# Kernel optimization log

Measured on AMD Instinct MI355X. Metric: run time of the kernel, lower is better.

## Reference

```python
import jax, jax.numpy as jnp
import numpy as np

N, C = 32768, 128
G, L = 64, 512
E = 524288
D_STATE, D_CONV, EXPAND = 16, 4, 2
D_INNER = EXPAND * C
DT_RANK = (C + 15) // 16  # ceil(d_model/16) = 8
EPS = 1e-5


def batch_norm(x, gamma, beta):
    # training-mode BatchNorm1d (batch statistics), eps=1e-5
    m = jnp.mean(x, axis=0)
    v = jnp.var(x, axis=0)
    return gamma * (x - m) * jax.lax.rsqrt(v + EPS) + beta


def mamba(h, in_W, conv_w, conv_b, xproj_W, dt_W, dt_b, A_log, Dp, out_W):
    # h: (G, L, C) dense-batched node features
    xz = h @ in_W                                   # (G, L, 2*D_INNER)
    xi, z = jnp.split(xz, 2, axis=-1)
    # causal depthwise conv1d (pad left d_conv-1), then SiLU
    xp = jnp.pad(xi, ((0, 0), (D_CONV - 1, 0), (0, 0)))
    xc = conv_b + sum(xp[:, k:k + L, :] * conv_w[:, k] for k in range(D_CONV))
    xc = jax.nn.silu(xc)                            # (G, L, D_INNER)
    proj = xc @ xproj_W                             # (G, L, DT_RANK + 2*D_STATE)
    dt_raw, Bm, Cm = jnp.split(proj, [DT_RANK, DT_RANK + D_STATE], axis=-1)
    dt = jax.nn.softplus(dt_raw @ dt_W + dt_b)      # (G, L, D_INNER)
    A = -jnp.exp(A_log)                             # (D_INNER, D_STATE)

    def step(hst, inp):
        dt_t, B_t, C_t, x_t = inp                   # (G,DI),(G,DS),(G,DS),(G,DI)
        dA = jnp.exp(dt_t[:, :, None] * A)          # (G, D_INNER, D_STATE)
        hst = hst * dA + (dt_t * x_t)[:, :, None] * B_t[:, None, :]
        y = jnp.einsum('gds,gs->gd', hst, C_t)
        return hst, y

    xs = (jnp.swapaxes(dt, 0, 1), jnp.swapaxes(Bm, 0, 1),
          jnp.swapaxes(Cm, 0, 1), jnp.swapaxes(xc, 0, 1))
    h0 = jnp.zeros((G, D_INNER, D_STATE), dt.dtype)
    _, ys = jax.lax.scan(step, h0, xs)              # ys: (L, G, D_INNER)
    y = jnp.swapaxes(ys, 0, 1) + xc * Dp
    y = y * jax.nn.silu(z)
    return y @ out_W                                # (G, L, C)


def setup_inputs() -> dict:
    key = jax.random.key(0)
    ks = jax.random.split(key, 16)
    s = 0.02
    rn = lambda k, shp: jax.random.normal(k, shp, jnp.float32) * s
    inp = {
        'x': jax.random.normal(ks[0], (N, C), jnp.float32),
        'edge_index': jax.random.randint(ks[1], (2, E), 0, N),
        'batch': jnp.arange(N) // L,  # 64 equal-size, sorted graphs
        # GraphConv (add-aggr): out = lin_rel(sum_j x_j) + lin_root(x)
        'W_root': rn(ks[2], (C, C)),
        'W_rel': rn(ks[3], (C, C)),
        'b_rel': jnp.zeros((C,), jnp.float32),
        # norm1/2/3 (BatchNorm1d)
        'n1_g': jnp.ones((C,), jnp.float32), 'n1_b': jnp.zeros((C,), jnp.float32),
        'n2_g': jnp.ones((C,), jnp.float32), 'n2_b': jnp.zeros((C,), jnp.float32),
        'n3_g': jnp.ones((C,), jnp.float32), 'n3_b': jnp.zeros((C,), jnp.float32),
        # MLP: BN -> Linear(C,2C) -> GELU -> BN -> Linear(2C,C)
        'mlp_bn1_g': jnp.ones((C,), jnp.float32), 'mlp_bn1_b': jnp.zeros((C,), jnp.float32),
        'mlp_W1': rn(ks[4], (C, 2 * C)), 'mlp_b1': jnp.zeros((2 * C,), jnp.float32),
        'mlp_bn2_g': jnp.ones((2 * C,), jnp.float32), 'mlp_bn2_b': jnp.zeros((2 * C,), jnp.float32),
        'mlp_W2': rn(ks[5], (2 * C, C)), 'mlp_b2': jnp.zeros((C,), jnp.float32),
        # Mamba params
        'in_W': rn(ks[6], (C, 2 * D_INNER)),
        'conv_w': rn(ks[7], (D_INNER, D_CONV)),
        'conv_b': jnp.zeros((D_INNER,), jnp.float32),
        'xproj_W': rn(ks[8], (D_INNER, DT_RANK + 2 * D_STATE)),
        'dt_W': rn(ks[9], (DT_RANK, D_INNER)),
        'dt_b': rn(ks[10], (D_INNER,)),
        'A_log': jnp.log(jnp.tile(jnp.arange(1, D_STATE + 1, dtype=jnp.float32), (D_INNER, 1))),
        'Dp': jnp.ones((D_INNER,), jnp.float32),
        'out_W': rn(ks[11], (D_INNER, C)),
    }
    return inp


def reference(x, edge_index, batch, W_root, W_rel, b_rel,
              n1_g, n1_b, n2_g, n2_b, n3_g, n3_b,
              mlp_bn1_g, mlp_bn1_b, mlp_W1, mlp_b1,
              mlp_bn2_g, mlp_bn2_b, mlp_W2, mlp_b2,
              in_W, conv_w, conv_b, xproj_W, dt_W, dt_b, A_log, Dp, out_W):
    src, dst = edge_index[0], edge_index[1]
    # conv branch (GraphConv, sum aggregation) + residual + norm1
    agg = jax.ops.segment_sum(x[src], dst, num_segments=N)
    h1 = agg @ W_rel + b_rel + x @ W_root + x
    h1 = batch_norm(h1, n1_g, n1_b)
    # mamba branch: to_dense_batch == reshape (batch = arange(N)//L, mask all-True)
    hd = x.reshape(G, L, C)
    y = mamba(hd, in_W, conv_w, conv_b, xproj_W, dt_W, dt_b, A_log, Dp, out_W).reshape(N, C)
    h2 = batch_norm(y + x, n2_g, n2_b)
    out = h1 + h2
    # gated MLP with internal batch norms (dropout is identity in eval)
    m = batch_norm(out, mlp_bn1_g, mlp_bn1_b) @ mlp_W1 + mlp_b1
    m = jax.nn.gelu(m, approximate=False)
    m = batch_norm(m, mlp_bn2_g, mlp_bn2_b) @ mlp_W2 + mlp_b2
    out = out + m
    return batch_norm(out, n3_g, n3_b)
```

## Files before the change

kernel.cpp:

```cpp
#include <hip/hip_runtime.h>


#define NROWS 32768
#define CDIM  128
#define EDGES 524288
#define GL    512
#define SCH   32
#define NCH   (GL / SCH)

typedef short s16x8 __attribute__((ext_vector_type(8)));
typedef float f32x4 __attribute__((ext_vector_type(4)));

__device__ __forceinline__ unsigned short f2bf(float f)
{
    unsigned u = __float_as_uint(f);
    u += 0x7FFF + ((u >> 16) & 1);
    return (unsigned short)(u >> 16);
}

__device__ __forceinline__ float bf2f(unsigned short u)
{
    return __uint_as_float((unsigned)u << 16);
}

__device__ __forceinline__ unsigned cvt_pk_bf16(float lo, float hi)
{
    unsigned r;
    asm("v_cvt_pk_bf16_f32 %0, %1, %2" : "=v"(r) : "v"(lo), "v"(hi));
    return r;
}

__device__ __forceinline__ float exp2_fast(float x)
{
    float r;
    asm("v_exp_f32 %0, %1" : "=v"(r) : "v"(x));
    return r;
}

__global__ __launch_bounds__(256) void k_hist(const int* __restrict__ ei,
                                              int* __restrict__ deg)
{
    const int e = blockIdx.x * 1024 + threadIdx.x * 4;
    const int4 d4 = *(const int4*)&ei[EDGES + e];
    atomicAdd(&deg[d4.x], 1);
    atomicAdd(&deg[d4.y], 1);
    atomicAdd(&deg[d4.z], 1);
    atomicAdd(&deg[d4.w], 1);
}

__global__ __launch_bounds__(1024) void k_scanidx(const int* __restrict__ deg,
                                                  int* __restrict__ base,
                                                  int* __restrict__ cursor)
{
    __shared__ int ps[1024];
    const int tid = threadIdx.x;
    int loc[32];
    int s = 0;
#pragma unroll
    for (int i = 0; i < 32; ++i) { loc[i] = deg[tid * 32 + i]; s += loc[i]; }
    ps[tid] = s;
    __syncthreads();
    for (int off = 1; off < 1024; off <<= 1) {
        int v = (tid >= off) ? ps[tid - off] : 0;
        __syncthreads();
        ps[tid] += v;
        __syncthreads();
    }
    int run = tid ? ps[tid - 1] : 0;
#pragma unroll
    for (int i = 0; i < 32; ++i) {
        base[tid * 32 + i] = run;
        cursor[tid * 32 + i] = run;
        run += loc[i];
    }
    if (tid == 0) base[32768] = EDGES;
}

__global__ __launch_bounds__(256) void k_fill(const int* __restrict__ ei,
                                              int* __restrict__ cursor,
                                              int* __restrict__ srcs)
{
    const int e = blockIdx.x * 1024 + threadIdx.x * 4;
    const int4 s4 = *(const int4*)&ei[e];
    const int4 d4 = *(const int4*)&ei[EDGES + e];
    int p;
    p = atomicAdd(&cursor[d4.x], 1); srcs[p] = s4.x;
    p = atomicAdd(&cursor[d4.y], 1); srcs[p] = s4.y;
    p = atomicAdd(&cursor[d4.z], 1); srcs[p] = s4.z;
    p = atomicAdd(&cursor[d4.w], 1); srcs[p] = s4.w;
}

__global__ __launch_bounds__(256) void k_gather(const float* __restrict__ x,
                                                const int* __restrict__ base,
                                                const int* __restrict__ srcs,
                                                float* __restrict__ agg)
{
    const int node = blockIdx.x * 4 + (threadIdx.x >> 6);
    const int lane = threadIdx.x & 63;
    const int b0 = base[node], b1 = base[node + 1];
    float2 a0 = make_float2(0.f, 0.f), a1 = make_float2(0.f, 0.f);
    int i = b0;
    for (; i + 2 <= b1; i += 2) {
        const int s0 = srcs[i], s1 = srcs[i + 1];
        const float2 v0 = *(const float2*)&x[(size_t)s0 * 128 + lane * 2];
        const float2 v1 = *(const float2*)&x[(size_t)s1 * 128 + lane * 2];
        a0.x += v0.x; a0.y += v0.y;
        a1.x += v1.x; a1.y += v1.y;
    }
    if (i < b1) {
        const int s0 = srcs[i];
        const float2 v0 = *(const float2*)&x[(size_t)s0 * 128 + lane * 2];
        a0.x += v0.x; a0.y += v0.y;
    }
    a0.x += a1.x; a0.y += a1.y;
    *(float2*)&agg[(size_t)node * 128 + lane * 2] = a0;
}

__global__ __launch_bounds__(256) void k_prepw5(
    const float* __restrict__ Wa, unsigned short* __restrict__ Ta,
    const float* __restrict__ Wb, unsigned short* __restrict__ Tb,
    const float* __restrict__ Wc, unsigned short* __restrict__ Tc,
    const float* __restrict__ Wd, unsigned short* __restrict__ Td,
    const float* __restrict__ We, unsigned short* __restrict__ Te)
{
    const int idx = blockIdx.x * 256 + threadIdx.x;
    const float* W; unsigned short* T; int rel, ks, N;
    if (idx < 16384)       { W = Wa; T = Ta; rel = idx;          ks = 7; N = 128; }
    else if (idx < 32768)  { W = Wb; T = Tb; rel = idx - 16384;  ks = 7; N = 128; }
    else if (idx < 98304)  { W = Wc; T = Tc; rel = idx - 32768;  ks = 7; N = 512; }
    else if (idx < 108544) { W = Wd; T = Td; rel = idx - 98304;  ks = 8; N = 40;  }
    else                   { W = We; T = Te; rel = idx - 108544; ks = 8; N = 128; }
    const int K = 1 << ks;
    const int n = rel >> ks, k = rel & (K - 1);
    T[rel] = f2bf(W[(size_t)k * N + n]);
}

template<bool DUAL, int ACT, bool STAT, bool ABF, bool OBF>
__global__ __launch_bounds__(256)
void gemm_mfma(const void* __restrict__ A0, const unsigned short* __restrict__ W0T,
               const void* __restrict__ A1p, const unsigned short* __restrict__ W1Tp,
               int M, int N, int K, int ldo,
               const float* __restrict__ bias,
               const float* __restrict__ resid, int ldr,
               void* __restrict__ outp,
               float* __restrict__ sumP, float* __restrict__ sqP)
{
    __shared__ __align__(16) unsigned short As[64 * 72];
    __shared__ __align__(16) unsigned short Bs[64 * 72];
    __shared__ float sB[2][64];

    const int tid = threadIdx.x;
    const int m0 = blockIdx.x * 64;
    const int n0 = blockIdx.y * 64;

    const int sr = tid >> 2;
    const int sk = (tid & 3) * 16;

    const int w  = tid >> 6, l = tid & 63;
    const int wr = (w >> 1) * 32, wc = (w & 1) * 32;
    const int fr = l & 15;
    const int fk = (l >> 4) * 8;

    f32x4 acc[2][2];
#pragma unroll
    for (int i = 0; i < 2; ++i)
#pragma unroll
        for (int j = 0; j < 2; ++j) acc[i][j] = (f32x4){0.f, 0.f, 0.f, 0.f};

    const int npass = DUAL ? 2 : 1;
    for (int pass = 0; pass < npass; ++pass) {
        const void* A = (DUAL && pass) ? A1p : A0;
        const unsigned short* WT = (DUAL && pass) ? W1Tp : W0T;
        for (int k0 = 0; k0 < K; k0 += 64) {
            if (ABF) {
                const unsigned short* ap =
                    (const unsigned short*)A + (size_t)(m0 + sr) * K + k0 + sk;
                *(uint4*)&As[sr * 72 + sk]     = *(const uint4*)(ap);
                *(uint4*)&As[sr * 72 + sk + 8] = *(const uint4*)(ap + 8);
            } else {
                const float* ap = (const float*)A + (size_t)(m0 + sr) * K + k0 + sk;
                float4 v0 = *(const float4*)(ap);
                float4 v1 = *(const float4*)(ap + 4);
                float4 v2 = *(const float4*)(ap + 8);
                float4 v3 = *(const float4*)(ap + 12);
                uint4 pa, pb;
                pa.x = cvt_pk_bf16(v0.x, v0.y); pa.y = cvt_pk_bf16(v0.z, v0.w);
                pa.z = cvt_pk_bf16(v1.x, v1.y); pa.w = cvt_pk_bf16(v1.z, v1.w);
                pb.x = cvt_pk_bf16(v2.x, v2.y); pb.y = cvt_pk_bf16(v2.z, v2.w);
                pb.z = cvt_pk_bf16(v3.x, v3.y); pb.w = cvt_pk_bf16(v3.z, v3.w);
                *(uint4*)&As[sr * 72 + sk]     = pa;
                *(uint4*)&As[sr * 72 + sk + 8] = pb;
            }
            {
                const int nn = n0 + sr;
                if (nn < N) {
                    const unsigned short* wp = WT + (size_t)nn * K + k0 + sk;
                    uint4 w0 = *(const uint4*)(wp);
                    uint4 w1 = *(const uint4*)(wp + 8);
                    *(uint4*)&Bs[sr * 72 + sk]     = w0;
                    *(uint4*)&Bs[sr * 72 + sk + 8] = w1;
                } else {
                    uint4 z = make_uint4(0, 0, 0, 0);
                    *(uint4*)&Bs[sr * 72 + sk]     = z;
                    *(uint4*)&Bs[sr * 72 + sk + 8] = z;
                }
            }
            __syncthreads();
#pragma unroll
            for (int ks = 0; ks < 2; ++ks) {
                s16x8 a0 = *(const s16x8*)&As[(wr + fr     ) * 72 + ks * 32 + fk];
                s16x8 a1 = *(const s16x8*)&As[(wr + 16 + fr) * 72 + ks * 32 + fk];
                s16x8 b0 = *(const s16x8*)&Bs[(wc + fr     ) * 72 + ks * 32 + fk];
                s16x8 b1 = *(const s16x8*)&Bs[(wc + 16 + fr) * 72 + ks * 32 + fk];
                acc[0][0] = __builtin_amdgcn_mfma_f32_16x16x32_bf16(a0, b0, acc[0][0], 0, 0, 0);
                acc[0][1] = __builtin_amdgcn_mfma_f32_16x16x32_bf16(a0, b1, acc[0][1], 0, 0, 0);
                acc[1][0] = __builtin_amdgcn_mfma_f32_16x16x32_bf16(a1, b0, acc[1][0], 0, 0, 0);
                acc[1][1] = __builtin_amdgcn_mfma_f32_16x16x32_bf16(a1, b1, acc[1][1], 0, 0, 0);
            }
            __syncthreads();
        }
    }

    const int orow = (l >> 4) * 4;
    float cs[2] = {0.f, 0.f}, cq[2] = {0.f, 0.f};
#pragma unroll
    for (int mt = 0; mt < 2; ++mt) {
#pragma unroll
        for (int nt = 0; nt < 2; ++nt) {
            const int cg = n0 + wc + nt * 16 + fr;
            if (cg < N) {
                const float bv = bias ? bias[cg] : 0.f;
#pragma unroll
                for (int r = 0; r < 4; ++r) {
                    const int rg = m0 + wr + mt * 16 + orow + r;
                    float v = acc[mt][nt][r] + bv;
                    if (resid) v += resid[(size_t)rg * ldr + cg];
                    if (ACT == 1)
                        v = 0.5f * v * (1.f + erff(v * 0.7071067811865475f));
                    if (OBF)
                        ((unsigned short*)outp)[(size_t)rg * ldo + cg] = f2bf(v);
                    else
                        ((float*)outp)[(size_t)rg * ldo + cg] = v;
                    if (STAT) { cs[nt] += v; cq[nt] += v * v; }
                }
            }
        }
    }
    if (STAT) {
        if (tid < 64) { sB[0][tid] = 0.f; sB[1][tid] = 0.f; }
        __syncthreads();
#pragma unroll
        for (int nt = 0; nt < 2; ++nt) {
            atomicAdd(&sB[0][wc + nt * 16 + fr], cs[nt]);
            atomicAdd(&sB[1][wc + nt * 16 + fr], cq[nt]);
        }
        __syncthreads();
        if (tid < 64 && (n0 + tid) < N) {
            atomicAdd(&sumP[n0 + tid], sB[0][tid]);
            atomicAdd(&sqP[n0 + tid],  sB[1][tid]);
        }
    }
}

__global__ __launch_bounds__(256) void k_conv(const unsigned short* __restrict__ xz,
                                              const float* __restrict__ cw,
                                              const float* __restrict__ cb,
                                              unsigned short* __restrict__ xc)
{
    const int r = blockIdx.x;
    const int l = r & (GL - 1);
    const int d = threadIdx.x;
    float4 w4 = *(const float4*)&cw[d * 4];
    const float taps[4] = {w4.x, w4.y, w4.z, w4.w};
    float acc = cb[d];
#pragma unroll
    for (int k = 0; k < 4; ++k) {
        int ll = l - 3 + k;
        if (ll >= 0) acc += bf2f(xz[(size_t)(r - 3 + k) * 512 + d]) * taps[k];
    }
    float s = 1.f / (1.f + __expf(-acc));
    xc[(size_t)r * 256 + d] = f2bf(acc * s);
}

__global__ __launch_bounds__(256) void k_dtbc(const float* __restrict__ proj,
                                              const float* __restrict__ dt_W,
                                              const float* __restrict__ dt_b,
                                              unsigned short* __restrict__ dtb,
                                              float* __restrict__ Bc,
                                              float* __restrict__ Cc)
{
    __shared__ float dtWS[8 * 256];
    __shared__ float dt_bS[256];
    __shared__ float projS[32 * 8];
    const int tid = threadIdx.x;
    const int r0 = blockIdx.x * 32;
    for (int i = tid; i < 2048; i += 256) dtWS[i] = dt_W[i];
    dt_bS[tid] = dt_b[tid];
    projS[tid] = proj[(size_t)(r0 + (tid >> 3)) * 40 + (tid & 7)];
    __syncthreads();

    const int c = tid;
    for (int rr = 0; rr < 32; ++rr) {
        float acc = dt_bS[c];
        const float* pr = &projS[rr * 8];
#pragma unroll
        for (int q = 0; q < 8; ++q) acc += pr[q] * dtWS[q * 256 + c];
        float e  = exp2_fast(-fabsf(acc) * 1.4426950408f);
        float sp = fmaxf(acc, 0.f) + 0.6931471806f * __log2f(1.f + e);
        dtb[(size_t)(r0 + rr) * 256 + c] = f2bf(sp);
    }
    for (int e2 = tid; e2 < 1024; e2 += 256) {
        int rr = e2 >> 5, cc = e2 & 31;
        float v = proj[(size_t)(r0 + rr) * 40 + 8 + cc];
        if (cc < 16) Bc[(size_t)(r0 + rr) * 16 + cc] = v;
        else         Cc[(size_t)(r0 + rr) * 16 + cc - 16] = v;
    }
}

__device__ __forceinline__ float dpp_add8(float x)
{
    float y = x;
    int t;
    t = __builtin_amdgcn_update_dpp(0, __float_as_int(y), 0xB1, 0xF, 0xF, true);
    y += __int_as_float(t);
    t = __builtin_amdgcn_update_dpp(0, __float_as_int(y), 0x4E, 0xF, 0xF, true);
    y += __int_as_float(t);
    t = __builtin_amdgcn_update_dpp(0, __float_as_int(y), 0x141, 0xF, 0xF, true);
    y += __int_as_float(t);
    return y;
}

__global__ __launch_bounds__(256) void k_scan(
    const unsigned short* __restrict__ dtb,
    const unsigned short* __restrict__ xcb,
    const unsigned short* __restrict__ xzb,
    const float* __restrict__ Bb, const float* __restrict__ Cb,
    const float* __restrict__ A_log, const float* __restrict__ Dp,
    unsigned short* __restrict__ yg)
{
    __shared__ __align__(16) float lds[2 * 3456 + 32 * 36];

    const int g    = blockIdx.x >> 3;
    const int dblk = blockIdx.x & 7;
    const int tid  = threadIdx.x;
    const int lane = tid & 63;
    const int dl   = (tid >> 6) * 8 + (lane >> 3);
    const int sp   = lane & 7;
    const int d0   = dblk * 32;
    const int d    = d0 + dl;
    const size_t rbase = (size_t)g * GL;

    const int sdd = tid & 31, stq = tid >> 5;
    const int sbt = tid >> 4, sbi = tid & 15;
    const int szt = tid >> 3, szi = tid & 7;

    const float L2E = 1.44269504088896f;
    const float aA0 = -__expf(A_log[d * 16 + 2 * sp]) * L2E;
    const float aA1 = -__expf(A_log[d * 16 + 2 * sp + 1]) * L2E;
    const float Dpd = Dp[d];
    float h0 = 0.f, h1 = 0.f;

    float rdt[4], rxc[4];
    float rB0, rB1, rC0, rC1;
    ushort4 rz, zcur;

    {
        const size_t r0 = rbase;
#pragma unroll
        for (int j = 0; j < 4; ++j) {
            rdt[j] = bf2f(dtb[(r0 + stq * 4 + j) * 256 + d0 + sdd]);
            rxc[j] = bf2f(xcb[(r0 + stq * 4 + j) * 256 + d0 + sdd]);
        }
        rz  = *(const ushort4*)&xzb[(r0 + szt) * 512 + 256 + d0 + szi * 4];
        rB0 = Bb[(r0 + sbt) * 16 + sbi];
        rB1 = Bb[(r0 + sbt + 16) * 16 + sbi];
        rC0 = Cb[(r0 + sbt) * 16 + sbi];
        rC1 = Cb[(r0 + sbt + 16) * 16 + sbi];
    }
    zcur = rz;

    float* ygL = lds + 2 * 3456;

    for (int c = 0; c < NCH; ++c) {
        float* buf = lds + (c & 1) * 3456;
        *(float4*)&buf[sdd * 36 + stq * 4] =
            make_float4(rdt[0], rdt[1], rdt[2], rdt[3]);
        *(float4*)&buf[1152 + sdd * 36 + stq * 4] =
            make_float4(rxc[0], rxc[1], rxc[2], rxc[3]);
        buf[2304 + sbi * 36 + sbt]      = rB0;
        buf[2304 + sbi * 36 + sbt + 16] = rB1;
        buf[2880 + sbi * 36 + sbt]      = rC0;
        buf[2880 + sbi * 36 + sbt + 16] = rC1;
        zcur = rz;
        __syncthreads();

        if (c + 1 < NCH) {
            const size_t r0 = rbase + (size_t)(c + 1) * SCH;
#pragma unroll
            for (int j = 0; j < 4; ++j) {
                rdt[j] = bf2f(dtb[(r0 + stq * 4 + j) * 256 + d0 + sdd]);
                rxc[j] = bf2f(xcb[(r0 + stq * 4 + j) * 256 + d0 + sdd]);
            }
            rz  = *(const ushort4*)&xzb[(r0 + szt) * 512 + 256 + d0 + szi * 4];
            rB0 = Bb[(r0 + sbt) * 16 + sbi];
            rB1 = Bb[(r0 + sbt + 16) * 16 + sbi];
            rC0 = Cb[(r0 + sbt) * 16 + sbi];
            rC1 = Cb[(r0 + sbt + 16) * 16 + sbi];
        }

        const float* pdt = buf + dl * 36;
        const float* pxc = buf + 1152 + dl * 36;
        const float* pB0 = buf + 2304 + (2 * sp) * 36;
        const float* pB1 = buf + 2304 + (2 * sp + 1) * 36;
        const float* pC0 = buf + 2880 + (2 * sp) * 36;
        const float* pC1 = buf + 2880 + (2 * sp + 1) * 36;
        float yk[4] = {0.f, 0.f, 0.f, 0.f};
#pragma unroll
        for (int t4 = 0; t4 < 8; ++t4) {
            const float4 dt4 = *(const float4*)&pdt[t4 * 4];
            const float4 xc4 = *(const float4*)&pxc[t4 * 4];
            const float4 B04 = *(const float4*)&pB0[t4 * 4];
            const float4 B14 = *(const float4*)&pB1[t4 * 4];
            const float4 C04 = *(const float4*)&pC0[t4 * 4];
            const float4 C14 = *(const float4*)&pC1[t4 * 4];
#define SSTEP(J)                                                            \
            {                                                               \
                const float dt = ((const float*)&dt4)[J];                   \
                const float xc = ((const float*)&xc4)[J];                   \
                const float dtx = dt * xc;                                  \
                h0 = h0 * exp2_fast(dt * aA0) + dtx * ((const float*)&B04)[J]; \
                h1 = h1 * exp2_fast(dt * aA1) + dtx * ((const float*)&B14)[J]; \
                float yv = h0 * ((const float*)&C04)[J]                     \
                         + h1 * ((const float*)&C14)[J];                    \
                yv = dpp_add8(yv);                                          \
                yv = fmaf(xc, Dpd, yv);                                     \
                const int tt = t4 * 4 + (J);                                \
                yk[t4 >> 1] = (sp == (tt & 7)) ? yv : yk[t4 >> 1];          \
            }
            SSTEP(0) SSTEP(1) SSTEP(2) SSTEP(3)
#undef SSTEP
        }
#pragma unroll
        for (int k = 0; k < 4; ++k)
            ygL[(k * 8 + sp) * 36 + dl] = yk[k];
        __syncthreads();

        {
            const size_t rr0 = rbase + (size_t)c * SCH;
            float4 y4 = *(const float4*)&ygL[szt * 36 + szi * 4];
            float z0 = bf2f(zcur.x), z1 = bf2f(zcur.y);
            float z2 = bf2f(zcur.z), z3 = bf2f(zcur.w);
            float o0 = y4.x * (z0 / (1.f + __expf(-z0)));
            float o1 = y4.y * (z1 / (1.f + __expf(-z1)));
            float o2 = y4.z * (z2 / (1.f + __expf(-z2)));
            float o3 = y4.w * (z3 / (1.f + __expf(-z3)));
            uint2 packed;
            packed.x = cvt_pk_bf16(o0, o1);
            packed.y = cvt_pk_bf16(o2, o3);
            *(uint2*)&yg[(rr0 + szt) * 256 + d0 + szi * 4] = packed;
        }
    }
}

__global__ __launch_bounds__(256) void k_add(const float* __restrict__ h1p,
                                             const float* __restrict__ p2,
                                             const float* __restrict__ st,
                                             const float* __restrict__ g1,
                                             const float* __restrict__ be1,
                                             const float* __restrict__ g2,
                                             const float* __restrict__ be2,
                                             float* __restrict__ outp,
                                             float* __restrict__ sumP,
                                             float* __restrict__ sqP)
{
    const int c = threadIdx.x & 127, half = threadIdx.x >> 7;
    const float inv = 1.f / 32768.f;
    const float m1 = st[c] * inv, v1 = st[128 + c] * inv - m1 * m1;
    const float a1 = g1[c] * rsqrtf(v1 + 1e-5f), b1 = be1[c] - m1 * a1;
    const float m2 = st[256 + c] * inv, v2 = st[384 + c] * inv - m2 * m2;
    const float a2 = g2[c] * rsqrtf(v2 + 1e-5f), b2 = be2[c] - m2 * a2;

    const int rbase = blockIdx.x * 64 + half * 32;
    float s = 0.f, q = 0.f;
    for (int i = 0; i < 32; ++i) {
        size_t idx = (size_t)(rbase + i) * 128 + c;
        float v = h1p[idx] * a1 + b1 + p2[idx] * a2 + b2;
        outp[idx] = v; s += v; q += v * v;
    }
    __shared__ float sh[2][2][128];
    sh[0][half][c] = s; sh[1][half][c] = q;
    __syncthreads();
    if (threadIdx.x < 128) {
        atomicAdd(&sumP[c], sh[0][0][c] + sh[0][1][c]);
        atomicAdd(&sqP[c],  sh[1][0][c] + sh[1][1][c]);
    }
}

__global__ __launch_bounds__(128) void k_fold1(
    const float* __restrict__ sumP, const float* __restrict__ sqP,
    const float* __restrict__ gam, const float* __restrict__ bet,
    const float* __restrict__ W1, const float* __restrict__ b1in,
    unsigned short* __restrict__ W1eT, float* __restrict__ b1e)
{
    __shared__ float red[128];
    const int n = blockIdx.x, k = threadIdx.x;
    const float inv = 1.f / 32768.f;
    const float m = sumP[k] * inv, v = sqP[k] * inv - m * m;
    const float a = gam[k] * rsqrtf(v + 1e-5f), bs = bet[k] - m * a;
    const float wv = W1[k * 256 + n];
    W1eT[n * 128 + k] = f2bf(a * wv);
    red[k] = bs * wv;
    __syncthreads();
    for (int s = 64; s > 0; s >>= 1) {
        if (k < s) red[k] += red[k + s];
        __syncthreads();
    }
    if (k == 0) b1e[n] = red[0] + b1in[n];
}

__global__ __launch_bounds__(256) void k_fold2(
    const float* __restrict__ sumP, const float* __restrict__ sqP,
    const float* __restrict__ gam, const float* __restrict__ bet,
    const float* __restrict__ W2, const float* __restrict__ b2in,
    unsigned short* __restrict__ W2eT, float* __restrict__ b2e)
{
    __shared__ float red[256];
    const int n = blockIdx.x, k = threadIdx.x;
    const float inv = 1.f / 32768.f;
    const float m = sumP[k] * inv, v = sqP[k] * inv - m * m;
    const float a = gam[k] * rsqrtf(v + 1e-5f), bs = bet[k] - m * a;
    const float wv = W2[k * 128 + n];
    W2eT[n * 256 + k] = f2bf(a * wv);
    red[k] = bs * wv;
    __syncthreads();
    for (int s = 128; s > 0; s >>= 1) {
        if (k < s) red[k] += red[k + s];
        __syncthreads();
    }
    if (k == 0) b2e[n] = red[0] + b2in[n];
}

__global__ __launch_bounds__(256) void k_bn3(const float* __restrict__ out2,
                                             const float* __restrict__ sumP,
                                             const float* __restrict__ sqP,
                                             const float* __restrict__ gam,
                                             const float* __restrict__ bet,
                                             float* __restrict__ dout)
{
    const int cq = (threadIdx.x & 31) * 4;
    const int rw = threadIdx.x >> 5;
    const float inv = 1.f / 32768.f;
    float a[4], b[4];
#pragma unroll
    for (int j = 0; j < 4; ++j) {
        float m = sumP[cq + j] * inv, v = sqP[cq + j] * inv - m * m;
        a[j] = gam[cq + j] * rsqrtf(v + 1e-5f);
        b[j] = bet[cq + j] - m * a[j];
    }
    const int r0 = blockIdx.x * 128 + rw;
#pragma unroll 4
    for (int k = 0; k < 16; ++k) {
        const size_t r = r0 + k * 8;
        float4 v = *(const float4*)&out2[r * 128 + cq];
        v.x = v.x * a[0] + b[0]; v.y = v.y * a[1] + b[1];
        v.z = v.z * a[2] + b[2]; v.w = v.w * a[3] + b[3];
        *(float4*)&dout[r * 128 + cq] = v;
    }
}

extern "C" void kernel_launch(void* const* d_in, const int* in_sizes, int n_in,
                              void* d_out, int out_size, void* d_ws, size_t ws_size,
                              hipStream_t stream)
{
    (void)in_sizes; (void)n_in; (void)out_size; (void)ws_size;
    const float* x      = (const float*)d_in[0];
    const int*   ei     = (const int*)d_in[1];
    const float* W_root = (const float*)d_in[3];
    const float* W_rel  = (const float*)d_in[4];
    const float* b_rel  = (const float*)d_in[5];
    const float* n1_g = (const float*)d_in[6],  *n1_b = (const float*)d_in[7];
    const float* n2_g = (const float*)d_in[8],  *n2_b = (const float*)d_in[9];
    const float* n3_g = (const float*)d_in[10], *n3_b = (const float*)d_in[11];
    const float* m1_g = (const float*)d_in[12], *m1_b = (const float*)d_in[13];
    const float* W1   = (const float*)d_in[14], *b1   = (const float*)d_in[15];
    const float* m2_g = (const float*)d_in[16], *m2_b = (const float*)d_in[17];
    const float* W2   = (const float*)d_in[18], *b2   = (const float*)d_in[19];
    const float* in_W   = (const float*)d_in[20];
    const float* conv_w = (const float*)d_in[21], *conv_b = (const float*)d_in[22];
    const float* xproj_W= (const float*)d_in[23];
    const float* dt_W   = (const float*)d_in[24], *dt_b = (const float*)d_in[25];
    const float* A_log  = (const float*)d_in[26], *Dp   = (const float*)d_in[27];
    const float* out_W  = (const float*)d_in[28];

    float* ws = (float*)d_ws;
    float* st  = ws;
    float* b1e = ws + 8192;
    float* b2e = ws + 8448;
    unsigned short* wsh   = (unsigned short*)(ws + 8704);
    unsigned short* WrelT  = wsh;
    unsigned short* WrootT = wsh + 16384;
    unsigned short* inWT   = wsh + 32768;
    unsigned short* xprojT = wsh + 98304;
    unsigned short* outWT  = wsh + 108544;
    unsigned short* W1eT   = wsh + 141312;
    unsigned short* W2eT   = wsh + 174080;
    float* big  = ws + 112640;
    float* agg  = big;
    float* p2   = agg;
    float* h1p  = big + 4194304;
    unsigned short* xz16  = (unsigned short*)(big + 8388608);
    unsigned short* xc16  = (unsigned short*)(big + 16777216);
    float* proj = big + 20971520;
    unsigned short* dtb16 = (unsigned short*)(big + 22282240);
    unsigned short* yg16  = dtb16;
    float* Bc   = big + 26476544;
    float* Cc   = big + 27000832;
    float* outb = big + 27525120;
    float* out2 = big + 31719424;
    unsigned short* g16   = (unsigned short*)(big + 35913728);

    int* ideg   = (int*)h1p;
    int* ibase  = ideg + 32768;
    int* icur   = ideg + 65552;
    int* isrcs  = ideg + 98320;

    hipMemsetAsync(st, 0, 2048 * sizeof(float), stream);
    hipMemsetAsync(ideg, 0, 32768 * sizeof(int), stream);

    k_prepw5<<<552, 256, 0, stream>>>(W_rel, WrelT, W_root, WrootT,
                                      in_W, inWT, xproj_W, xprojT,
                                      out_W, outWT);

    k_hist<<<512, 256, 0, stream>>>(ei, ideg);
    k_scanidx<<<1, 1024, 0, stream>>>(ideg, ibase, icur);
    k_fill<<<512, 256, 0, stream>>>(ei, icur, isrcs);
    k_gather<<<8192, 256, 0, stream>>>(x, ibase, isrcs, agg);

    gemm_mfma<true, 0, true, false, false><<<dim3(512, 2), 256, 0, stream>>>(
        agg, WrelT, x, WrootT, NROWS, 128, 128, 128,
        b_rel, x, 128, h1p, st + 0, st + 128);
    gemm_mfma<false, 0, false, false, true><<<dim3(512, 8), 256, 0, stream>>>(
        x, inWT, nullptr, nullptr, NROWS, 512, 128, 512,
        nullptr, nullptr, 0, xz16, nullptr, nullptr);
    k_conv<<<32768, 256, 0, stream>>>(xz16, conv_w, conv_b, xc16);
    gemm_mfma<false, 0, false, true, false><<<dim3(512, 1), 256, 0, stream>>>(
        xc16, xprojT, nullptr, nullptr, NROWS, 40, 256, 40,
        nullptr, nullptr, 0, proj, nullptr, nullptr);
    k_dtbc<<<1024, 256, 0, stream>>>(proj, dt_W, dt_b, dtb16, Bc, Cc);
    k_scan<<<512, 256, 0, stream>>>(dtb16, xc16, xz16, Bc, Cc, A_log, Dp, yg16);
    gemm_mfma<false, 0, true, true, false><<<dim3(512, 2), 256, 0, stream>>>(
        yg16, outWT, nullptr, nullptr, NROWS, 128, 256, 128,
        nullptr, x, 128, p2, st + 256, st + 384);
    k_add<<<512, 256, 0, stream>>>(h1p, p2, st, n1_g, n1_b, n2_g, n2_b,
                                   outb, st + 512, st + 640);
    k_fold1<<<256, 128, 0, stream>>>(st + 512, st + 640, m1_g, m1_b, W1, b1, W1eT, b1e);
    gemm_mfma<false, 1, true, false, true><<<dim3(512, 4), 256, 0, stream>>>(
        outb, W1eT, nullptr, nullptr, NROWS, 256, 128, 256,
        b1e, nullptr, 0, g16, st + 768, st + 1024);
    k_fold2<<<128, 256, 0, stream>>>(st + 768, st + 1024, m2_g, m2_b, W2, b2, W2eT, b2e);
    gemm_mfma<false, 0, true, true, false><<<dim3(512, 2), 256, 0, stream>>>(
        g16, W2eT, nullptr, nullptr, NROWS, 128, 256, 128,
        b2e, outb, 128, out2, st + 1280, st + 1408);
    k_bn3<<<256, 256, 0, stream>>>(out2, st + 1280, st + 1408, n3_g, n3_b,
                                   (float*)d_out);
}
```

Baseline: 393.5 us.

## Store x, aggregates and pre-norm intermediates in bf16; split scan into smaller blocks

Adds a pass that converts x to bf16 once. The neighbour gather and the GEMMs then read bf16 inputs, and the gather writes bf16 aggregates. The h1 and p2 intermediates are also stored as bf16 and read back in the add/batch-norm kernel, which halves the traffic for those buffers. Separately, the scan kernel moves to 128-thread blocks covering 16 channels each, using 4x more blocks, with B/C staged into LDS through vectorized loads. The trade-off is lower precision in the aggregation sum and the pre-BN activations, plus an extra conversion kernel.

```diff
diff --git a/kernel.cpp b/kernel.cpp
--- a/kernel.cpp
+++ b/kernel.cpp
@@ -90,30 +90,34 @@
     p = atomicAdd(&cursor[d4.w], 1); srcs[p] = s4.w;
 }
 
-__global__ __launch_bounds__(256) void k_gather(const float* __restrict__ x,
+__global__ __launch_bounds__(256) void k_prepx(const float* __restrict__ x,
+                                               unsigned short* __restrict__ x16)
+{
+    const size_t i = ((size_t)blockIdx.x * 256 + threadIdx.x) * 8;
+    float4 a = *(const float4*)&x[i];
+    float4 b = *(const float4*)&x[i + 4];
+    uint4 p;
+    p.x = cvt_pk_bf16(a.x, a.y); p.y = cvt_pk_bf16(a.z, a.w);
+    p.z = cvt_pk_bf16(b.x, b.y); p.w = cvt_pk_bf16(b.z, b.w);
+    *(uint4*)&x16[i] = p;
+}
+
+__global__ __launch_bounds__(256) void k_gather(const unsigned short* __restrict__ x16,
                                                 const int* __restrict__ base,
                                                 const int* __restrict__ srcs,
-                                                float* __restrict__ agg)
+                                                unsigned short* __restrict__ agg16)
 {
     const int node = blockIdx.x * 4 + (threadIdx.x >> 6);
     const int lane = threadIdx.x & 63;
     const int b0 = base[node], b1 = base[node + 1];
-    float2 a0 = make_float2(0.f, 0.f), a1 = make_float2(0.f, 0.f);
-    int i = b0;
-    for (; i + 2 <= b1; i += 2) {
-        const int s0 = srcs[i], s1 = srcs[i + 1];
-        const float2 v0 = *(const float2*)&x[(size_t)s0 * 128 + lane * 2];
-        const float2 v1 = *(const float2*)&x[(size_t)s1 * 128 + lane * 2];
-        a0.x += v0.x; a0.y += v0.y;
-        a1.x += v1.x; a1.y += v1.y;
-    }
-    if (i < b1) {
-        const int s0 = srcs[i];
-        const float2 v0 = *(const float2*)&x[(size_t)s0 * 128 + lane * 2];
-        a0.x += v0.x; a0.y += v0.y;
-    }
-    a0.x += a1.x; a0.y += a1.y;
-    *(float2*)&agg[(size_t)node * 128 + lane * 2] = a0;
+    float a0 = 0.f, a1 = 0.f;
+    for (int i = b0; i < b1; ++i) {
+        const int s = srcs[i];
+        const unsigned v = *(const unsigned*)&x16[(size_t)s * 128 + lane * 2];
+        a0 += bf2f((unsigned short)(v & 0xFFFF));
+        a1 += bf2f((unsigned short)(v >> 16));
+    }
+    *(unsigned*)&agg16[(size_t)node * 128 + lane * 2] = cvt_pk_bf16(a0, a1);
 }
 
 __global__ __launch_bounds__(256) void k_prepw5(
@@ -330,7 +334,7 @@
     return y;
 }
 
-__global__ __launch_bounds__(256) void k_scan(
+__global__ __launch_bounds__(128) void k_scan(
     const unsigned short* __restrict__ dtb,
     const unsigned short* __restrict__ xcb,
     const unsigned short* __restrict__ xzb,
@@ -338,21 +342,20 @@
     const float* __restrict__ A_log, const float* __restrict__ Dp,
     unsigned short* __restrict__ yg)
 {
-    __shared__ __align__(16) float lds[2 * 3456 + 32 * 36];
-
-    const int g    = blockIdx.x >> 3;
-    const int dblk = blockIdx.x & 7;
+    __shared__ __align__(16) float lds[2 * 2304 + 32 * 20];
+
+    const int g    = blockIdx.x >> 5;
+    const int dblk = blockIdx.x & 31;
     const int tid  = threadIdx.x;
     const int lane = tid & 63;
     const int dl   = (tid >> 6) * 8 + (lane >> 3);
     const int sp   = lane & 7;
-    const int d0   = dblk * 32;
+    const int d0   = dblk * 16;
     const int d    = d0 + dl;
     const size_t rbase = (size_t)g * GL;
 
-    const int sdd = tid & 31, stq = tid >> 5;
-    const int sbt = tid >> 4, sbi = tid & 15;
-    const int szt = tid >> 3, szi = tid & 7;
+    const int sdd = tid & 15, stq = tid >> 4;
+    const int szt = tid >> 2, szi = tid & 3;
 
     const float L2E = 1.44269504088896f;
     const float aA0 = -__expf(A_log[d * 16 + 2 * sp]) * L2E;
@@ -360,37 +363,35 @@
     const float Dpd = Dp[d];
     float h0 = 0.f, h1 = 0.f;
 
-    float rdt[4], rxc[4];
-    float rB0, rB1, rC0, rC1;
+    float rdt[4], rxc[4], rB[4], rC[4];
     ushort4 rz, zcur;
 
     {
         const size_t r0 = rbase;
 #pragma unroll
         for (int j = 0; j < 4; ++j) {
-            rdt[j] = bf2f(dtb[(r0 + stq * 4 + j) * 256 + d0 + sdd]);
-            rxc[j] = bf2f(xcb[(r0 + stq * 4 + j) * 256 + d0 + sdd]);
-        }
-        rz  = *(const ushort4*)&xzb[(r0 + szt) * 512 + 256 + d0 + szi * 4];
-        rB0 = Bb[(r0 + sbt) * 16 + sbi];
-        rB1 = Bb[(r0 + sbt + 16) * 16 + sbi];
-        rC0 = Cb[(r0 + sbt) * 16 + sbi];
-        rC1 = Cb[(r0 + sbt + 16) * 16 + sbi];
+            const size_t row = r0 + stq * 4 + j;
+            rdt[j] = bf2f(dtb[row * 256 + d0 + sdd]);
+            rxc[j] = bf2f(xcb[row * 256 + d0 + sdd]);
+            rB[j]  = Bb[row * 16 + sdd];
+            rC[j]  = Cb[row * 16 + sdd];
+        }
+        rz = *(const ushort4*)&xzb[(r0 + szt) * 512 + 256 + d0 + szi * 4];
     }
     zcur = rz;
 
-    float* ygL = lds + 2 * 3456;
+    float* ygL = lds + 2 * 2304;
 
     for (int c = 0; c < NCH; ++c) {
-        float* buf = lds + (c & 1) * 3456;
+        float* buf = lds + (c & 1) * 2304;
         *(float4*)&buf[sdd * 36 + stq * 4] =
             make_float4(rdt[0], rdt[1], rdt[2], rdt[3]);
+        *(float4*)&buf[576 + sdd * 36 + stq * 4] =
+            make_float4(rxc[0], rxc[1], rxc[2], rxc[3]);
         *(float4*)&buf[1152 + sdd * 36 + stq * 4] =
-            make_float4(rxc[0], rxc[1], rxc[2], rxc[3]);
-        buf[2304 + sbi * 36 + sbt]      = rB0;
-        buf[2304 + sbi * 36 + sbt + 16] = rB1;
-        buf[2880 + sbi * 36 + sbt]      = rC0;
-        buf[2880 + sbi * 36 + sbt + 16] = rC1;
+            make_float4(rB[0], rB[1], rB[2], rB[3]);
+        *(float4*)&buf[1728 + sdd * 36 + stq * 4] =
+            make_float4(rC[0], rC[1], rC[2], rC[3]);
         zcur = rz;
         __syncthreads();
 
@@ -398,22 +399,21 @@
             const size_t r0 = rbase + (size_t)(c + 1) * SCH;
 #pragma unroll
             for (int j = 0; j < 4; ++j) {
-                rdt[j] = bf2f(dtb[(r0 + stq * 4 + j) * 256 + d0 + sdd]);
-                rxc[j] = bf2f(xcb[(r0 + stq * 4 + j) * 256 + d0 + sdd]);
+                const size_t row = r0 + stq * 4 + j;
+                rdt[j] = bf2f(dtb[row * 256 + d0 + sdd]);
+                rxc[j] = bf2f(xcb[row * 256 + d0 + sdd]);
+                rB[j]  = Bb[row * 16 + sdd];
+                rC[j]  = Cb[row * 16 + sdd];
             }
-            rz  = *(const ushort4*)&xzb[(r0 + szt) * 512 + 256 + d0 + szi * 4];
-            rB0 = Bb[(r0 + sbt) * 16 + sbi];
-            rB1 = Bb[(r0 + sbt + 16) * 16 + sbi];
-            rC0 = Cb[(r0 + sbt) * 16 + sbi];
-            rC1 = Cb[(r0 + sbt + 16) * 16 + sbi];
+            rz = *(const ushort4*)&xzb[(r0 + szt) * 512 + 256 + d0 + szi * 4];
         }
 
         const float* pdt = buf + dl * 36;
-        const float* pxc = buf + 1152 + dl * 36;
-        const float* pB0 = buf + 2304 + (2 * sp) * 36;
-        const float* pB1 = buf + 2304 + (2 * sp + 1) * 36;
-        const float* pC0 = buf + 2880 + (2 * sp) * 36;
-        const float* pC1 = buf + 2880 + (2 * sp + 1) * 36;
+        const float* pxc = buf + 576 + dl * 36;
+        const float* pB0 = buf + 1152 + (2 * sp) * 36;
+        const float* pB1 = buf + 1152 + (2 * sp + 1) * 36;
+        const float* pC0 = buf + 1728 + (2 * sp) * 36;
+        const float* pC1 = buf + 1728 + (2 * sp + 1) * 36;
         float yk[4] = {0.f, 0.f, 0.f, 0.f};
 #pragma unroll
         for (int t4 = 0; t4 < 8; ++t4) {
@@ -442,12 +442,12 @@
         }
 #pragma unroll
         for (int k = 0; k < 4; ++k)
-            ygL[(k * 8 + sp) * 36 + dl] = yk[k];
+            ygL[(k * 8 + sp) * 20 + dl] = yk[k];
         __syncthreads();
 
         {
             const size_t rr0 = rbase + (size_t)c * SCH;
-            float4 y4 = *(const float4*)&ygL[szt * 36 + szi * 4];
+            float4 y4 = *(const float4*)&ygL[szt * 20 + szi * 4];
             float z0 = bf2f(zcur.x), z1 = bf2f(zcur.y);
             float z2 = bf2f(zcur.z), z3 = bf2f(zcur.w);
             float o0 = y4.x * (z0 / (1.f + __expf(-z0)));
@@ -462,8 +462,8 @@
     }
 }
 
-__global__ __launch_bounds__(256) void k_add(const float* __restrict__ h1p,
-                                             const float* __restrict__ p2,
+__global__ __launch_bounds__(256) void k_add(const unsigned short* __restrict__ h1p,
+                                             const unsigned short* __restrict__ p2,
                                              const float* __restrict__ st,
                                              const float* __restrict__ g1,
                                              const float* __restrict__ be1,
@@ -484,7 +484,7 @@
     float s = 0.f, q = 0.f;
     for (int i = 0; i < 32; ++i) {
         size_t idx = (size_t)(rbase + i) * 128 + c;
-        float v = h1p[idx] * a1 + b1 + p2[idx] * a2 + b2;
+        float v = bf2f(h1p[idx]) * a1 + b1 + bf2f(p2[idx]) * a2 + b2;
         outp[idx] = v; s += v; q += v * v;
     }
     __shared__ float sh[2][2][128];
@@ -604,22 +604,23 @@
     unsigned short* outWT  = wsh + 108544;
     unsigned short* W1eT   = wsh + 141312;
     unsigned short* W2eT   = wsh + 174080;
-    float* big  = ws + 112640;
-    float* agg  = big;
-    float* p2   = agg;
-    float* h1p  = big + 4194304;
-    unsigned short* xz16  = (unsigned short*)(big + 8388608);
-    unsigned short* xc16  = (unsigned short*)(big + 16777216);
-    float* proj = big + 20971520;
-    unsigned short* dtb16 = (unsigned short*)(big + 22282240);
+    float* big = ws + 112640;
+    unsigned short* agg16 = (unsigned short*)(big);
+    unsigned short* p216  = agg16;
+    unsigned short* h1p16 = (unsigned short*)(big + 2097152);
+    unsigned short* x16   = (unsigned short*)(big + 4194304);
+    unsigned short* xz16  = (unsigned short*)(big + 6291456);
+    unsigned short* xc16  = (unsigned short*)(big + 14680064);
+    float* proj = big + 18874368;
+    unsigned short* dtb16 = (unsigned short*)(big + 20185088);
     unsigned short* yg16  = dtb16;
-    float* Bc   = big + 26476544;
-    float* Cc   = big + 27000832;
-    float* outb = big + 27525120;
-    float* out2 = big + 31719424;
-    unsigned short* g16   = (unsigned short*)(big + 35913728);
-
-    int* ideg   = (int*)h1p;
+    float* Bc   = big + 24379392;
+    float* Cc   = big + 24903680;
+    float* outb = big + 25427968;
+    float* out2 = big + 29622272;
+    unsigned short* g16   = (unsigned short*)(big + 33816576);
+
+    int* ideg   = (int*)h1p16;
     int* ibase  = ideg + 32768;
     int* icur   = ideg + 65552;
     int* isrcs  = ideg + 98320;
@@ -630,28 +631,29 @@
     k_prepw5<<<552, 256, 0, stream>>>(W_rel, WrelT, W_root, WrootT,
                                       in_W, inWT, xproj_W, xprojT,
                                       out_W, outWT);
+    k_prepx<<<2048, 256, 0, stream>>>(x, x16);
 
     k_hist<<<512, 256, 0, stream>>>(ei, ideg);
     k_scanidx<<<1, 1024, 0, stream>>>(ideg, ibase, icur);
     k_fill<<<512, 256, 0, stream>>>(ei, icur, isrcs);
-    k_gather<<<8192, 256, 0, stream>>>(x, ibase, isrcs, agg);
-
-    gemm_mfma<true, 0, true, false, false><<<dim3(512, 2), 256, 0, stream>>>(
-        agg, WrelT, x, WrootT, NROWS, 128, 128, 128,
-        b_rel, x, 128, h1p, st + 0, st + 128);
-    gemm_mfma<false, 0, false, false, true><<<dim3(512, 8), 256, 0, stream>>>(
-        x, inWT, nullptr, nullptr, NROWS, 512, 128, 512,
+    k_gather<<<8192, 256, 0, stream>>>(x16, ibase, isrcs, agg16);
+
+    gemm_mfma<true, 0, true, true, true><<<dim3(512, 2), 256, 0, stream>>>(
+        agg16, WrelT, x16, WrootT, NROWS, 128, 128, 128,
+        b_rel, x, 128, h1p16, st + 0, st + 128);
+    gemm_mfma<false, 0, false, true, true><<<dim3(512, 8), 256, 0, stream>>>(
+        x16, inWT, nullptr, nullptr, NROWS, 512, 128, 512,
         nullptr, nullptr, 0, xz16, nullptr, nullptr);
     k_conv<<<32768, 256, 0, stream>>>(xz16, conv_w, conv_b, xc16);
     gemm_mfma<false, 0, false, true, false><<<dim3(512, 1), 256, 0, stream>>>(
         xc16, xprojT, nullptr, nullptr, NROWS, 40, 256, 40,
         nullptr, nullptr, 0, proj, nullptr, nullptr);
     k_dtbc<<<1024, 256, 0, stream>>>(proj, dt_W, dt_b, dtb16, Bc, Cc);
-    k_scan<<<512, 256, 0, stream>>>(dtb16, xc16, xz16, Bc, Cc, A_log, Dp, yg16);
-    gemm_mfma<false, 0, true, true, false><<<dim3(512, 2), 256, 0, stream>>>(
+    k_scan<<<2048, 128, 0, stream>>>(dtb16, xc16, xz16, Bc, Cc, A_log, Dp, yg16);
+    gemm_mfma<false, 0, true, true, true><<<dim3(512, 2), 256, 0, stream>>>(
         yg16, outWT, nullptr, nullptr, NROWS, 128, 256, 128,
-        nullptr, x, 128, p2, st + 256, st + 384);
-    k_add<<<512, 256, 0, stream>>>(h1p, p2, st, n1_g, n1_b, n2_g, n2_b,
+        nullptr, x, 128, p216, st + 256, st + 384);
+    k_add<<<512, 256, 0, stream>>>(h1p16, p216, st, n1_g, n1_b, n2_g, n2_b,
                                    outb, st + 512, st + 640);
     k_fold1<<<256, 128, 0, stream>>>(st + 512, st + 640, m1_g, m1_b, W1, b1, W1eT, b1e);
     gemm_mfma<false, 1, true, false, true><<<dim3(512, 4), 256, 0, stream>>>(
```

Measured after the change: 452.6 us. +15.0%, slower.
